# Kernel optimization log

Measured on AMD Instinct MI355X. Metric: run time of the kernel, lower is better.

## Reference

```python
import jax, jax.numpy as jnp
import numpy as np

N = 100000      # nodes (single ntype 'paper' for the reference)
R = 4           # relations
E = 300000      # edges per relation
P = 2           # prediction relations (pred_in_n_rev_etypes)
FEAT = 64       # feat_len
H = 64          # gen_h_dim
B = 2           # num_bases
NUM_PRED = 5
S = 4096        # seed nodes


def setup_inputs() -> dict:
    key = jax.random.key(0)
    ks = jax.random.split(key, 26)
    sc = 0.05
    inp = {
        "x": jax.random.normal(ks[0], (N, FEAT), jnp.float32),
        "edges": jax.random.randint(ks[1], (R, E, 2), 0, N, dtype=jnp.int32),
        "seeds": jax.random.randint(ks[2], (S,), 0, N, dtype=jnp.int32),
        "noise": jax.random.normal(ks[3], (N, H), jnp.float32),
        # RelGraphConv layer 1 (basis decomposition) and layer 2
        "V1": jax.random.normal(ks[4], (B, FEAT, H), jnp.float32) * sc,
        "C1": jax.random.normal(ks[5], (R, B), jnp.float32) * sc,
        "V2": jax.random.normal(ks[6], (B, H, H), jnp.float32) * sc,
        "C2": jax.random.normal(ks[7], (R, B), jnp.float32) * sc,
        # per-ntype linear head
        "W_lin": jax.random.normal(ks[8], (H, H), jnp.float32) * sc,
        "b_lin": jnp.zeros((H,), jnp.float32),
        # ReldGen per-relation MLP: H->256->32->1
        "Wd1": jax.random.normal(ks[9], (P, H, 256), jnp.float32) * sc,
        "bd1": jnp.zeros((P, 256), jnp.float32),
        "Wd2": jax.random.normal(ks[10], (P, 256, 32), jnp.float32) * sc,
        "bd2": jnp.zeros((P, 32), jnp.float32),
        "Wd3": jax.random.normal(ks[11], (P, 32, 1), jnp.float32) * sc,
        "bd3": jnp.zeros((P, 1), jnp.float32),
        # RelfGen per-relation MLP: H->256->2048->NUM_PRED*FEAT
        "Wf1": jax.random.normal(ks[12], (P, H, 256), jnp.float32) * sc,
        "bf1": jnp.zeros((P, 256), jnp.float32),
        "Wf2": jax.random.normal(ks[13], (P, 256, 2048), jnp.float32) * sc,
        "bf2": jnp.zeros((P, 2048), jnp.float32),
        "Wf3": jax.random.normal(ks[14], (P, 2048, NUM_PRED * FEAT), jnp.float32) * sc,
        "bf3": jnp.zeros((P, NUM_PRED * FEAT), jnp.float32),
    }
    return inp


def _rel_conv(h, V, C, edges):
    # basis decomposition: W_r = sum_b C[r,b] * V[b]
    Wr = jnp.einsum('rb,bio->rio', C, V)          # [R, in, out]
    m = jnp.einsum('ni,rio->rno', h, Wr)           # transform-then-gather

    def per_rel(m_r, e_r):
        msg = m_r[e_r[:, 0]]                       # gather src  [E, out]
        agg = jax.ops.segment_sum(msg, e_r[:, 1], num_segments=N)
        deg = jax.ops.segment_sum(jnp.ones((e_r.shape[0],), m_r.dtype),
                                  e_r[:, 1], num_segments=N)
        return agg / jnp.maximum(deg, 1.0)[:, None]  # GraphConv norm='right'

    out = jax.vmap(per_rel)(m, edges)              # [R, N, out]
    return jax.nn.relu(out.sum(axis=0))            # HeteroGraphConv 'sum' + relu


def reference(x, edges, seeds, noise, V1, C1, V2, C2, W_lin, b_lin,
              Wd1, bd1, Wd2, bd2, Wd3, bd3, Wf1, bf1, Wf2, bf2, Wf3, bf3):
    h = _rel_conv(x, V1, C1, edges)                # layer 1: FEAT -> H
    h = _rel_conv(h, V2, C2, edges)                # layer 2: H -> H
    h = jax.nn.leaky_relu(h @ W_lin + b_lin)       # per-ntype linear head
    h = h + noise                                  # Sampler: h + N(0,1)
    hs = h[seeds]                                  # [S, H]
    # ReldGen: predicted missing-neighbor counts per relation
    d = jax.nn.leaky_relu(jnp.einsum('sh,phk->psk', hs, Wd1) + bd1[:, None, :])
    d = jax.nn.leaky_relu(jnp.einsum('psk,pkm->psm', d, Wd2) + bd2[:, None, :])
    pred_missing = jax.nn.relu(jnp.einsum('psm,pmo->pso', d, Wd3) + bd3[:, None, :])  # [P,S,1]
    # RelfGen: predicted neighbor features per relation
    f = jax.nn.relu(jnp.einsum('sh,phk->psk', hs, Wf1) + bf1[:, None, :])
    f = jax.nn.relu(jnp.einsum('psk,pkm->psm', f, Wf2) + bf2[:, None, :])
    f = jnp.tanh(jnp.einsum('psm,pmo->pso', f, Wf3) + bf3[:, None, :])
    pred_feat = f.reshape(P, S, NUM_PRED, FEAT)
    return pred_missing, pred_feat
```

## Files before the change

kernel.cpp:

```cpp
#include <hip/hip_runtime.h>
#include <math.h>

#define NN 100000
#define RR 4
#define EE 300000
#define PP 2
#define HH 64
#define SS 4096
#define NSEG (NN * RR)
#define FPART 8
#define PWIDTH ((NN + FPART - 1) / FPART)

typedef __attribute__((ext_vector_type(8))) short short8;
typedef __attribute__((ext_vector_type(4))) short short4v;
typedef __attribute__((ext_vector_type(4))) float f32x4;

__device__ __forceinline__ short f2bf(float v) {
    unsigned u = __float_as_uint(v);
    unsigned r = (u + 0x7FFFu + ((u >> 16) & 1u)) >> 16;
    return (short)r;
}
__device__ __forceinline__ float bf2f(short s) {
    return __uint_as_float(((unsigned)(unsigned short)s) << 16);
}
__device__ __forceinline__ float bflo(unsigned v) { return __uint_as_float(v << 16); }
__device__ __forceinline__ float bfhi(unsigned v) { return __uint_as_float(v & 0xFFFF0000u); }

__global__ void compute_wr_t2(const float* __restrict__ C1, const float* __restrict__ V1,
                              short* __restrict__ hi1, short* __restrict__ lo1,
                              const float* __restrict__ C2, const float* __restrict__ V2,
                              short* __restrict__ hi2, short* __restrict__ lo2) {
    int b = blockIdx.x;
    const float* C = (b < 64) ? C1 : C2;
    const float* V = (b < 64) ? V1 : V2;
    short* hi = (b < 64) ? hi1 : hi2;
    short* lo = (b < 64) ? lo1 : lo2;
    int idx = (b & 63) * 256 + threadIdx.x;
    int o = idx >> 8;
    int ri = idx & 255;
    int r = ri >> 6;
    int i = ri & 63;
    float v = C[r * 2] * V[i * 64 + o] + C[r * 2 + 1] * V[4096 + i * 64 + o];
    short h = f2bf(v);
    hi[idx] = h;
    lo[idx] = f2bf(v - bf2f(h));
}

struct PrepPtrs {
    const float *Wlin, *Wd1, *Wd2, *Wf1, *Wf2, *Wf3;
    short *Wlin_hi, *Wlin_lo, *Wd1_hi, *Wd1_lo, *Wd2_hi, *Wd2_lo,
          *Wf1_hi, *Wf1_lo, *Wf2_hi, *Wf2_lo, *Wf3_hi, *Wf3_lo;
};

__device__ __forceinline__ void tsp_one(const float* __restrict__ W, short* __restrict__ hi,
                                        short* __restrict__ lo, int K, int N, int idx) {
    int total = K * N;
    int z = idx / total;
    int rem = idx - z * total;
    int n = rem / K;
    int k = rem - n * K;
    float v = W[(long long)z * total + (long long)k * N + n];
    short h = f2bf(v);
    hi[idx] = h;
    lo[idx] = f2bf(v - bf2f(h));
}

#define T0 4096
#define T1 32768
#define T2 16384
#define T3 32768
#define T4 1048576
#define T5 1310720
#define TSP_TOTAL (T0 + T1 + T2 + T3 + T4 + T5)

__global__ void prep_weights(PrepPtrs pp) {
    int idx = blockIdx.x * 256 + threadIdx.x;
    if (idx >= TSP_TOTAL) return;
    if (idx < T0) { tsp_one(pp.Wlin, pp.Wlin_hi, pp.Wlin_lo, 64, 64, idx); return; }
    idx -= T0;
    if (idx < T1) { tsp_one(pp.Wd1, pp.Wd1_hi, pp.Wd1_lo, 64, 256, idx); return; }
    idx -= T1;
    if (idx < T2) { tsp_one(pp.Wd2, pp.Wd2_hi, pp.Wd2_lo, 256, 32, idx); return; }
    idx -= T2;
    if (idx < T3) { tsp_one(pp.Wf1, pp.Wf1_hi, pp.Wf1_lo, 64, 256, idx); return; }
    idx -= T3;
    if (idx < T4) { tsp_one(pp.Wf2, pp.Wf2_hi, pp.Wf2_lo, 256, 2048, idx); return; }
    idx -= T4;
    tsp_one(pp.Wf3, pp.Wf3_hi, pp.Wf3_lo, 2048, 320, idx);
}

__global__ void to_bf16(const float* __restrict__ x, short* __restrict__ xb, int n4) {
    int idx = blockIdx.x * 256 + threadIdx.x;
    if (idx >= n4) return;
    f32x4 v = *(const f32x4*)&x[(long long)idx * 4];
    short4v o;
    #pragma unroll
    for (int c = 0; c < 4; c++) o[c] = f2bf(v[c]);
    *(short4v*)&xb[(long long)idx * 4] = o;
}

__global__ void count_kernel(const int* __restrict__ edges, int* __restrict__ counts) {
    int idx = blockIdx.x * 256 + threadIdx.x;
    if (idx >= RR * EE) return;
    int r = idx / EE;
    int dst = edges[2 * idx + 1];
    atomicAdd(&counts[dst * RR + r], 1);
}

__global__ void scan1(const int* __restrict__ counts, int* __restrict__ excl,
                      int* __restrict__ bsums, int n) {
    __shared__ int tmp[256];
    int tid = threadIdx.x;
    int gid = blockIdx.x * 256 + tid;
    int v = (gid < n) ? counts[gid] : 0;
    tmp[tid] = v;
    __syncthreads();
    #pragma unroll
    for (int off = 1; off < 256; off <<= 1) {
        int y = (tid >= off) ? tmp[tid - off] : 0;
        __syncthreads();
        tmp[tid] += y;
        __syncthreads();
    }
    if (gid < n) excl[gid] = tmp[tid] - v;
    if (tid == 255) bsums[blockIdx.x] = tmp[255];
}

__global__ void scan2(int* __restrict__ bsums, int nb) {
    __shared__ int tmp[256];
    __shared__ int carry;
    int tid = threadIdx.x;
    if (tid == 0) carry = 0;
    __syncthreads();
    for (int base = 0; base < nb; base += 256) {
        int i = base + tid;
        int v = (i < nb) ? bsums[i] : 0;
        tmp[tid] = v;
        __syncthreads();
        #pragma unroll
        for (int off = 1; off < 256; off <<= 1) {
            int y = (tid >= off) ? tmp[tid - off] : 0;
            __syncthreads();
            tmp[tid] += y;
            __syncthreads();
        }
        if (i < nb) bsums[i] = tmp[tid] - v + carry;
        __syncthreads();
        if (tid == 0) carry += tmp[255];
        __syncthreads();
    }
}

__global__ void scan3(const int* __restrict__ excl, const int* __restrict__ bsums,
                      int* __restrict__ row_ptr, int* __restrict__ cursor, int n, int total) {
    int gid = blockIdx.x * 256 + threadIdx.x;
    if (gid < n) {
        int v = excl[gid] + bsums[gid >> 8];
        row_ptr[gid] = v;
        cursor[gid] = v;
    }
    if (gid == 0) row_ptr[n] = total;
}

__global__ void fill_csr(const int* __restrict__ edges, int* __restrict__ cursor,
                         int* __restrict__ csr_src) {
    int part = blockIdx.x & (FPART - 1);
    int idx = (blockIdx.x >> 3) * 256 + threadIdx.x;
    if (idx >= RR * EE) return;
    int dst = edges[2 * idx + 1];
    int lo = part * PWIDTH;
    if (dst < lo || dst >= lo + PWIDTH) return;
    int r = idx / EE;
    int src = edges[2 * idx];
    int pos = atomicAdd(&cursor[dst * RR + r], 1);
    csr_src[pos] = src;
}

__global__ __launch_bounds__(256) void gather_agg(const int* __restrict__ row_ptr,
                                                  const int* __restrict__ csr_src,
                                                  const short* __restrict__ feat,
                                                  short* __restrict__ agg) {
    long long tg = (long long)blockIdx.x * 256 + threadIdx.x;
    long long seg = tg >> 5;
    int cl = threadIdx.x & 31;
    if (seg >= (long long)NSEG) return;
    int beg = row_ptr[seg];
    int end = row_ptr[seg + 1];
    float s0 = 0.f, s1 = 0.f;
    int i = beg;
    for (; i + 4 <= end; i += 4) {
        int a = csr_src[i];
        int b = csr_src[i + 1];
        int c = csr_src[i + 2];
        int d = csr_src[i + 3];
        unsigned va = *(const unsigned*)&feat[a * HH + cl * 2];
        unsigned vb = *(const unsigned*)&feat[b * HH + cl * 2];
        unsigned vc = *(const unsigned*)&feat[c * HH + cl * 2];
        unsigned vd = *(const unsigned*)&feat[d * HH + cl * 2];
        s0 += (bflo(va) + bflo(vb)) + (bflo(vc) + bflo(vd));
        s1 += (bfhi(va) + bfhi(vb)) + (bfhi(vc) + bfhi(vd));
    }
    int rem = end - i;
    if (rem > 0) {
        int a = csr_src[i];
        int b = csr_src[rem > 1 ? i + 1 : i];
        int c = csr_src[rem > 2 ? i + 2 : i];
        unsigned va = *(const unsigned*)&feat[a * HH + cl * 2];
        unsigned vb = *(const unsigned*)&feat[b * HH + cl * 2];
        unsigned vc = *(const unsigned*)&feat[c * HH + cl * 2];
        s0 += bflo(va);
        s1 += bfhi(va);
        s0 += (rem > 1) ? bflo(vb) : 0.f;
        s1 += (rem > 1) ? bfhi(vb) : 0.f;
        s0 += (rem > 2) ? bflo(vc) : 0.f;
        s1 += (rem > 2) ? bfhi(vc) : 0.f;
    }
    int d = end - beg;
    float inv = 1.0f / (float)(d > 1 ? d : 1);
    unsigned plo = (unsigned)(unsigned short)f2bf(s0 * inv);
    unsigned phi = (unsigned)(unsigned short)f2bf(s1 * inv);
    *(unsigned*)&agg[seg * HH + cl * 2] = plo | (phi << 16);
}

__global__ void gather_kernel(const float* __restrict__ h, const int* __restrict__ seeds,
                              float* __restrict__ hs) {
    int idx = blockIdx.x * 256 + threadIdx.x;
    if (idx >= SS * HH) return;
    int s = idx >> 6;
    hs[idx] = h[(long long)seeds[s] * HH + (idx & 63)];
}

__global__ void d3_kernel(const float* __restrict__ d2v, const float* __restrict__ Wd3,
                          const float* __restrict__ bd3, float* __restrict__ out) {
    int idx = blockIdx.x * 256 + threadIdx.x;
    if (idx >= PP * SS) return;
    int p = idx >> 12;
    const float* row = d2v + (long long)idx * 32;
    const float* w = Wd3 + p * 32;
    float s = bd3[p];
    #pragma unroll
    for (int k = 0; k < 32; k++) s += row[k] * w[k];
    out[idx] = fmaxf(s, 0.f);
}

__global__ void reduce_tanh(const float* __restrict__ part, const float* __restrict__ bf3,
                            float* __restrict__ out) {
    int idx = blockIdx.x * 256 + threadIdx.x;
    if (idx >= PP * SS * 320) return;
    int p = idx / (SS * 320);
    int rem = idx - p * (SS * 320);
    int n = rem % 320;
    float s = bf3[p * 320 + n];
    #pragma unroll
    for (int ks = 0; ks < 4; ks++)
        s += part[((long long)(p * 4 + ks)) * SS * 320 + rem];
    out[idx] = tanhf(s);
}

__global__ __launch_bounds__(256) void head1_gemm(
    const float* __restrict__ hs,
    const short* __restrict__ Bd_hi, const short* __restrict__ Bd_lo, const float* __restrict__ bd,
    const short* __restrict__ Bf_hi, const short* __restrict__ Bf_lo, const float* __restrict__ bfb,
    short* __restrict__ outd, short* __restrict__ outf)
{
    __shared__ short As_hi[128 * 32];
    __shared__ short As_lo[128 * 32];
    __shared__ short Bs_hi[64 * 32];
    __shared__ short Bs_lo[64 * 32];

    int z = blockIdx.z;
    int head = z >> 1, p = z & 1;
    const short* Bhi = (head ? Bf_hi : Bd_hi) + (long long)p * 256 * 64;
    const short* Blo = (head ? Bf_lo : Bd_lo) + (long long)p * 256 * 64;
    const float* bz = (head ? bfb : bd) + p * 256;
    short* Cc = (head ? outf : outd) + (long long)p * SS * 256;

    int m0 = blockIdx.y * 128;
    int n0 = blockIdx.x * 64;
    int tid = threadIdx.x;
    int lane = tid & 63;
    int w = tid >> 6;
    int wm = w >> 1, wn = w & 1;
    int mrow = lane & 15;
    int quad = lane >> 4;

    f32x4 acc[4][2];
    #pragma unroll
    for (int s = 0; s < 4; s++)
        #pragma unroll
        for (int t = 0; t < 2; t++)
            acc[s][t] = (f32x4){0.f, 0.f, 0.f, 0.f};

    #pragma unroll
    for (int k0 = 0; k0 < 64; k0 += 32) {
        #pragma unroll
        for (int i = 0; i < 4; i++) {
            int f = tid + i * 256;
            int m = f >> 3, k4 = f & 7;
            f32x4 v = *(const f32x4*)&hs[(m0 + m) * 64 + k0 + k4 * 4];
            short4v hv, lv;
            #pragma unroll
            for (int c = 0; c < 4; c++) {
                short hh = f2bf(v[c]);
                hv[c] = hh;
                lv[c] = f2bf(v[c] - bf2f(hh));
            }
            *(short4v*)&As_hi[m * 32 + k4 * 4] = hv;
            *(short4v*)&As_lo[m * 32 + k4 * 4] = lv;
        }
        {
            int n = tid >> 2, q = tid & 3;
            long long boff = (long long)(n0 + n) * 64 + k0 + q * 8;
            *(short8*)&Bs_hi[n * 32 + q * 8] = *(const short8*)&Bhi[boff];
            *(short8*)&Bs_lo[n * 32 + q * 8] = *(const short8*)&Blo[boff];
        }
        __syncthreads();

        short8 ah[4], al[4], bh[2], bl[2];
        #pragma unroll
        for (int s = 0; s < 4; s++) {
            int soff = (wm * 64 + s * 16 + mrow) * 32 + quad * 8;
            ah[s] = *(const short8*)&As_hi[soff];
            al[s] = *(const short8*)&As_lo[soff];
        }
        #pragma unroll
        for (int t = 0; t < 2; t++) {
            int soff = (wn * 32 + t * 16 + mrow) * 32 + quad * 8;
            bh[t] = *(const short8*)&Bs_hi[soff];
            bl[t] = *(const short8*)&Bs_lo[soff];
        }
        #pragma unroll
        for (int s = 0; s < 4; s++)
            #pragma unroll
            for (int t = 0; t < 2; t++) {
                acc[s][t] = __builtin_amdgcn_mfma_f32_16x16x32_bf16(ah[s], bh[t], acc[s][t], 0, 0, 0);
                acc[s][t] = __builtin_amdgcn_mfma_f32_16x16x32_bf16(ah[s], bl[t], acc[s][t], 0, 0, 0);
                acc[s][t] = __builtin_amdgcn_mfma_f32_16x16x32_bf16(al[s], bh[t], acc[s][t], 0, 0, 0);
            }
        __syncthreads();
    }

    #pragma unroll
    for (int s = 0; s < 4; s++) {
        int gmBase = m0 + wm * 64 + s * 16 + quad * 4;
        #pragma unroll
        for (int t = 0; t < 2; t++) {
            int gn = n0 + wn * 32 + t * 16 + mrow;
            float bb = bz[gn];
            #pragma unroll
            for (int r = 0; r < 4; r++) {
                int gm = gmBase + r;
                float v = acc[s][t][r] + bb;
                v = (head == 1) ? fmaxf(v, 0.f) : ((v > 0.f) ? v : 0.01f * v);
                Cc[(long long)gm * 256 + gn] = f2bf(v);
            }
        }
    }
}

template <int ACT, bool ADD, bool OUTBF, int KSPLIT>
__global__ __launch_bounds__(256) void mfma_gemm_bfA(
    const short* __restrict__ A, int lda, long long sA,
    const short* __restrict__ Bhi, const short* __restrict__ Blo, long long sB,
    const float* __restrict__ bias, long long sBias,
    const float* __restrict__ Dadd,
    void* __restrict__ Cc, int ldc, long long sC,
    int M, int Nn, int K)
{
    __shared__ short As[128 * 32];
    __shared__ short Bs_hi[64 * 32];
    __shared__ short Bs_lo[64 * 32];

    int z = blockIdx.z;
    int p = z / KSPLIT, ks = z % KSPLIT;
    A += (long long)p * sA;
    Bhi += (long long)p * sB;
    Blo += (long long)p * sB;
    const float* bz = bias ? bias + (long long)p * sBias : nullptr;
    long long cbase = (long long)((KSPLIT > 1) ? z : p) * sC;

    int Kc = K / KSPLIT;
    int kbeg = ks * Kc;

    int m0 = blockIdx.y * 128;
    int n0 = blockIdx.x * 64;
    int tid = threadIdx.x;
    int lane = tid & 63;
    int w = tid >> 6;
    int wm = w >> 1, wn = w & 1;
    int mrow = lane & 15;
    int quad = lane >> 4;

    f32x4 acc[4][2];
    #pragma unroll
    for (int s = 0; s < 4; s++)
        #pragma unroll
        for (int t = 0; t < 2; t++)
            acc[s][t] = (f32x4){0.f, 0.f, 0.f, 0.f};

    for (int k0 = kbeg; k0 < kbeg + Kc; k0 += 32) {
        #pragma unroll
        for (int i = 0; i < 2; i++) {
            int f = tid + i * 256;
            int m = f >> 2, q = f & 3;
            int gm = m0 + m;
            short8 av = (short8)0;
            if (gm < M) av = *(const short8*)&A[(long long)gm * lda + k0 + q * 8];
            *(short8*)&As[m * 32 + q * 8] = av;
        }
        {
            int n = tid >> 2, q = tid & 3;
            int gn = n0 + n;
            short8 bh = (short8)0, bl = (short8)0;
            if (gn < Nn) {
                long long boff = (long long)gn * K + k0 + q * 8;
                bh = *(const short8*)&Bhi[boff];
                bl = *(const short8*)&Blo[boff];
            }
            *(short8*)&Bs_hi[n * 32 + q * 8] = bh;
            *(short8*)&Bs_lo[n * 32 + q * 8] = bl;
        }
        __syncthreads();

        short8 ah[4], bh[2], bl[2];
        #pragma unroll
        for (int s = 0; s < 4; s++)
            ah[s] = *(const short8*)&As[(wm * 64 + s * 16 + mrow) * 32 + quad * 8];
        #pragma unroll
        for (int t = 0; t < 2; t++) {
            int soff = (wn * 32 + t * 16 + mrow) * 32 + quad * 8;
            bh[t] = *(const short8*)&Bs_hi[soff];
            bl[t] = *(const short8*)&Bs_lo[soff];
        }
        #pragma unroll
        for (int s = 0; s < 4; s++)
            #pragma unroll
            for (int t = 0; t < 2; t++) {
                acc[s][t] = __builtin_amdgcn_mfma_f32_16x16x32_bf16(ah[s], bh[t], acc[s][t], 0, 0, 0);
                acc[s][t] = __builtin_amdgcn_mfma_f32_16x16x32_bf16(ah[s], bl[t], acc[s][t], 0, 0, 0);
            }
        __syncthreads();
    }

    #pragma unroll
    for (int s = 0; s < 4; s++) {
        int gmBase = m0 + wm * 64 + s * 16 + quad * 4;
        #pragma unroll
        for (int t = 0; t < 2; t++) {
            int gn = n0 + wn * 32 + t * 16 + mrow;
            if (gn >= Nn) continue;
            float bb = bz ? bz[gn] : 0.f;
            #pragma unroll
            for (int r = 0; r < 4; r++) {
                int gm = gmBase + r;
                if (gm >= M) continue;
                float v = acc[s][t][r] + bb;
                if (ACT == 1) v = fmaxf(v, 0.f);
                else if (ACT == 2) v = (v > 0.f) ? v : 0.01f * v;
                else if (ACT == 3) v = tanhf(v);
                if (ADD) v += Dadd[(long long)gm * ldc + gn];
                long long co = cbase + (long long)gm * ldc + gn;
                if (OUTBF) ((short*)Cc)[co] = f2bf(v);
                else ((float*)Cc)[co] = v;
            }
        }
    }
}

extern "C" void kernel_launch(void* const* d_in, const int* in_sizes, int n_in,
                              void* d_out, int out_size, void* d_ws, size_t ws_size,
                              hipStream_t stream) {
    const float* x    = (const float*)d_in[0];
    const int* edges  = (const int*)d_in[1];
    const int* seeds  = (const int*)d_in[2];
    const float* noise= (const float*)d_in[3];
    const float* V1   = (const float*)d_in[4];
    const float* C1   = (const float*)d_in[5];
    const float* V2   = (const float*)d_in[6];
    const float* C2   = (const float*)d_in[7];
    const float* Wlin = (const float*)d_in[8];
    const float* blin = (const float*)d_in[9];
    const float* Wd1 = (const float*)d_in[10]; const float* bd1 = (const float*)d_in[11];
    const float* Wd2 = (const float*)d_in[12]; const float* bd2 = (const float*)d_in[13];
    const float* Wd3 = (const float*)d_in[14]; const float* bd3 = (const float*)d_in[15];
    const float* Wf1 = (const float*)d_in[16]; const float* bf1 = (const float*)d_in[17];
    const float* Wf2 = (const float*)d_in[18]; const float* bf2 = (const float*)d_in[19];
    const float* Wf3 = (const float*)d_in[20]; const float* bf3 = (const float*)d_in[21];

    float* out = (float*)d_out;

    char* ws = (char*)d_ws;
    size_t off = 0;
    auto allocf = [&](size_t nf) {
        float* p = (float*)(ws + off);
        off += ((nf * 4 + 255) / 256) * 256;
        return p;
    };
    auto allocs = [&](size_t ns) {
        short* p = (short*)(ws + off);
        off += ((ns * 2 + 255) / 256) * 256;
        return p;
    };
    auto alloci = [&](size_t ni) {
        int* p = (int*)(ws + off);
        off += ((ni * 4 + 255) / 256) * 256;
        return p;
    };

    short* Wrt1_hi = allocs(16384);          short* Wrt1_lo = allocs(16384);
    short* Wrt2_hi = allocs(16384);          short* Wrt2_lo = allocs(16384);
    short* Wlint_hi = allocs(4096);          short* Wlint_lo = allocs(4096);
    short* Wd1t_hi = allocs(2 * 64 * 256);   short* Wd1t_lo = allocs(2 * 64 * 256);
    short* Wd2t_hi = allocs(2 * 256 * 32);   short* Wd2t_lo = allocs(2 * 256 * 32);
    short* Wf1t_hi = allocs(2 * 64 * 256);   short* Wf1t_lo = allocs(2 * 64 * 256);
    short* Wf2t_hi = allocs((size_t)2 * 256 * 2048);  short* Wf2t_lo = allocs((size_t)2 * 256 * 2048);
    short* Wf3t_hi = allocs((size_t)2 * 2048 * 320);  short* Wf3t_lo = allocs((size_t)2 * 2048 * 320);

    int* counts  = alloci(NSEG);
    int* excl    = alloci(NSEG);
    int* bsums   = alloci(2048);
    int* row_ptr = alloci(NSEG + 1);
    int* cursor  = alloci(NSEG);
    int* csr_src = alloci((size_t)RR * EE);

    short* xb  = allocs((size_t)NN * HH);
    short* agg = allocs((size_t)NSEG * HH);
    short* h1  = allocs((size_t)NN * HH);
    short* h2  = allocs((size_t)NN * HH);
    float* h3  = allocf((size_t)NN * HH);
    float* hs  = allocf((size_t)SS * HH);
    short* d1b = allocs((size_t)PP * SS * 256);
    float* d2v = allocf((size_t)PP * SS * 32);
    short* f1  = allocs((size_t)PP * SS * 256);
    short* f2b = allocs((size_t)PP * SS * 2048);

    float* fpart = (float*)agg;

    compute_wr_t2<<<128, 256, 0, stream>>>(C1, V1, Wrt1_hi, Wrt1_lo, C2, V2, Wrt2_hi, Wrt2_lo);
    PrepPtrs pp;
    pp.Wlin = Wlin; pp.Wd1 = Wd1; pp.Wd2 = Wd2; pp.Wf1 = Wf1; pp.Wf2 = Wf2; pp.Wf3 = Wf3;
    pp.Wlin_hi = Wlint_hi; pp.Wlin_lo = Wlint_lo;
    pp.Wd1_hi = Wd1t_hi;   pp.Wd1_lo = Wd1t_lo;
    pp.Wd2_hi = Wd2t_hi;   pp.Wd2_lo = Wd2t_lo;
    pp.Wf1_hi = Wf1t_hi;   pp.Wf1_lo = Wf1t_lo;
    pp.Wf2_hi = Wf2t_hi;   pp.Wf2_lo = Wf2t_lo;
    pp.Wf3_hi = Wf3t_hi;   pp.Wf3_lo = Wf3t_lo;
    prep_weights<<<(TSP_TOTAL + 255) / 256, 256, 0, stream>>>(pp);

    to_bf16<<<(NN * HH / 4 + 255) / 256, 256, 0, stream>>>(x, xb, NN * HH / 4);

    hipMemsetAsync(counts, 0, (size_t)NSEG * 4, stream);
    int eb0 = (RR * EE + 255) / 256;
    count_kernel<<<eb0, 256, 0, stream>>>(edges, counts);
    int nb = (NSEG + 255) / 256;
    scan1<<<nb, 256, 0, stream>>>(counts, excl, bsums, NSEG);
    scan2<<<1, 256, 0, stream>>>(bsums, nb);
    scan3<<<nb, 256, 0, stream>>>(excl, bsums, row_ptr, cursor, NSEG, RR * EE);
    fill_csr<<<eb0 * FPART, 256, 0, stream>>>(edges, cursor, csr_src);

    int gb = (int)(((long long)NSEG * 32 + 255) / 256);
    int MY = (NN + 127) / 128;

    gather_agg<<<gb, 256, 0, stream>>>(row_ptr, csr_src, xb, agg);
    mfma_gemm_bfA<1, false, true, 1><<<dim3(1, MY, 1), 256, 0, stream>>>(
        agg, 256, 0, Wrt1_hi, Wrt1_lo, 0, nullptr, 0, nullptr,
        h1, 64, 0, NN, 64, 256);

    gather_agg<<<gb, 256, 0, stream>>>(row_ptr, csr_src, h1, agg);
    mfma_gemm_bfA<1, false, true, 1><<<dim3(1, MY, 1), 256, 0, stream>>>(
        agg, 256, 0, Wrt2_hi, Wrt2_lo, 0, nullptr, 0, nullptr,
        h2, 64, 0, NN, 64, 256);

    mfma_gemm_bfA<2, true, false, 1><<<dim3(1, MY, 1), 256, 0, stream>>>(
        h2, 64, 0, Wlint_hi, Wlint_lo, 0, blin, 0, noise,
        h3, 64, 0, NN, 64, 64);

    gather_kernel<<<(SS * HH + 255) / 256, 256, 0, stream>>>(h3, seeds, hs);

    head1_gemm<<<dim3(4, 32, 4), 256, 0, stream>>>(
        hs, Wd1t_hi, Wd1t_lo, bd1, Wf1t_hi, Wf1t_lo, bf1, d1b, f1);

    mfma_gemm_bfA<2, false, false, 1><<<dim3(1, 32, PP), 256, 0, stream>>>(
        d1b, 256, (long long)SS * 256, Wd2t_hi, Wd2t_lo, (long long)32 * 256, bd2, 32, nullptr,
        d2v, 32, (long long)SS * 32, SS, 32, 256);
    d3_kernel<<<(PP * SS + 255) / 256, 256, 0, stream>>>(d2v, Wd3, bd3, out);

    mfma_gemm_bfA<1, false, true, 1><<<dim3(32, 32, PP), 256, 0, stream>>>(
        f1, 256, (long long)SS * 256, Wf2t_hi, Wf2t_lo, (long long)2048 * 256, bf2, 2048, nullptr,
        f2b, 2048, (long long)SS * 2048, SS, 2048, 256);
    mfma_gemm_bfA<0, false, false, 4><<<dim3(5, 32, PP * 4), 256, 0, stream>>>(
        f2b, 2048, (long long)SS * 2048, Wf3t_hi, Wf3t_lo, (long long)320 * 2048, nullptr, 0, nullptr,
        fpart, 320, (long long)SS * 320, SS, 320, 2048);
    reduce_tanh<<<(PP * SS * 320 + 255) / 256, 256, 0, stream>>>(fpart, bf3, out + (size_t)PP * SS);
}
```

Baseline: 572.3 us.

## Fuse prep kernels, layer-2 GEMM with linear head, and d-head layers; widen gather loads

Three preprocessing kernels (basis weight combine, weight transpose/split, x to bf16) become one launch. The layer-2 relation GEMM is fused with the linear head, leaky ReLU and noise add through shared memory, so the h2 round trip disappears. The seed gather moves into head1, and the Wd2 GEMM is fused with the final Wd3 dot product. gather_agg now has 16 lanes per segment, each loading 8 bytes instead of 4. Together these cut launches and intermediate global traffic, at the cost of more shared memory per block in the fused kernels.

```diff
diff --git a/kernel.cpp b/kernel.cpp
--- a/kernel.cpp
+++ b/kernel.cpp
@@ -14,6 +14,7 @@
 typedef __attribute__((ext_vector_type(8))) short short8;
 typedef __attribute__((ext_vector_type(4))) short short4v;
 typedef __attribute__((ext_vector_type(4))) float f32x4;
+typedef __attribute__((ext_vector_type(2))) unsigned int u32x2;
 
 __device__ __forceinline__ short f2bf(float v) {
     unsigned u = __float_as_uint(v);
@@ -25,31 +26,18 @@
 }
 __device__ __forceinline__ float bflo(unsigned v) { return __uint_as_float(v << 16); }
 __device__ __forceinline__ float bfhi(unsigned v) { return __uint_as_float(v & 0xFFFF0000u); }
-
-__global__ void compute_wr_t2(const float* __restrict__ C1, const float* __restrict__ V1,
-                              short* __restrict__ hi1, short* __restrict__ lo1,
-                              const float* __restrict__ C2, const float* __restrict__ V2,
-                              short* __restrict__ hi2, short* __restrict__ lo2) {
-    int b = blockIdx.x;
-    const float* C = (b < 64) ? C1 : C2;
-    const float* V = (b < 64) ? V1 : V2;
-    short* hi = (b < 64) ? hi1 : hi2;
-    short* lo = (b < 64) ? lo1 : lo2;
-    int idx = (b & 63) * 256 + threadIdx.x;
-    int o = idx >> 8;
-    int ri = idx & 255;
-    int r = ri >> 6;
-    int i = ri & 63;
-    float v = C[r * 2] * V[i * 64 + o] + C[r * 2 + 1] * V[4096 + i * 64 + o];
-    short h = f2bf(v);
-    hi[idx] = h;
-    lo[idx] = f2bf(v - bf2f(h));
+__device__ __forceinline__ unsigned pack2(float a, float b) {
+    return (unsigned)(unsigned short)f2bf(a) | ((unsigned)(unsigned short)f2bf(b) << 16);
 }
 
 struct PrepPtrs {
     const float *Wlin, *Wd1, *Wd2, *Wf1, *Wf2, *Wf3;
     short *Wlin_hi, *Wlin_lo, *Wd1_hi, *Wd1_lo, *Wd2_hi, *Wd2_lo,
           *Wf1_hi, *Wf1_lo, *Wf2_hi, *Wf2_lo, *Wf3_hi, *Wf3_lo;
+    const float *C1, *V1, *C2, *V2;
+    short *wr1_hi, *wr1_lo, *wr2_hi, *wr2_lo;
+    const float *x;
+    short *xb;
 };
 
 __device__ __forceinline__ void tsp_one(const float* __restrict__ W, short* __restrict__ hi,
@@ -72,31 +60,51 @@
 #define T4 1048576
 #define T5 1310720
 #define TSP_TOTAL (T0 + T1 + T2 + T3 + T4 + T5)
-
-__global__ void prep_weights(PrepPtrs pp) {
-    int idx = blockIdx.x * 256 + threadIdx.x;
-    if (idx >= TSP_TOTAL) return;
-    if (idx < T0) { tsp_one(pp.Wlin, pp.Wlin_hi, pp.Wlin_lo, 64, 64, idx); return; }
-    idx -= T0;
-    if (idx < T1) { tsp_one(pp.Wd1, pp.Wd1_hi, pp.Wd1_lo, 64, 256, idx); return; }
-    idx -= T1;
-    if (idx < T2) { tsp_one(pp.Wd2, pp.Wd2_hi, pp.Wd2_lo, 256, 32, idx); return; }
-    idx -= T2;
-    if (idx < T3) { tsp_one(pp.Wf1, pp.Wf1_hi, pp.Wf1_lo, 64, 256, idx); return; }
-    idx -= T3;
-    if (idx < T4) { tsp_one(pp.Wf2, pp.Wf2_hi, pp.Wf2_lo, 256, 2048, idx); return; }
-    idx -= T4;
-    tsp_one(pp.Wf3, pp.Wf3_hi, pp.Wf3_lo, 2048, 320, idx);
-}
-
-__global__ void to_bf16(const float* __restrict__ x, short* __restrict__ xb, int n4) {
-    int idx = blockIdx.x * 256 + threadIdx.x;
-    if (idx >= n4) return;
-    f32x4 v = *(const f32x4*)&x[(long long)idx * 4];
+#define WR_BLK 128
+#define TSP_BLK 9552
+#define XB_BLK 6250
+
+__global__ void prep_all(PrepPtrs pp) {
+    int b = blockIdx.x;
+    if (b < WR_BLK) {
+        const float* C = (b < 64) ? pp.C1 : pp.C2;
+        const float* V = (b < 64) ? pp.V1 : pp.V2;
+        short* hi = (b < 64) ? pp.wr1_hi : pp.wr2_hi;
+        short* lo = (b < 64) ? pp.wr1_lo : pp.wr2_lo;
+        int idx = (b & 63) * 256 + threadIdx.x;
+        int o = idx >> 8;
+        int ri = idx & 255;
+        int r = ri >> 6;
+        int i = ri & 63;
+        float v = C[r * 2] * V[i * 64 + o] + C[r * 2 + 1] * V[4096 + i * 64 + o];
+        short h = f2bf(v);
+        hi[idx] = h;
+        lo[idx] = f2bf(v - bf2f(h));
+        return;
+    }
+    b -= WR_BLK;
+    if (b < TSP_BLK) {
+        int idx = b * 256 + threadIdx.x;
+        if (idx < T0) { tsp_one(pp.Wlin, pp.Wlin_hi, pp.Wlin_lo, 64, 64, idx); return; }
+        idx -= T0;
+        if (idx < T1) { tsp_one(pp.Wd1, pp.Wd1_hi, pp.Wd1_lo, 64, 256, idx); return; }
+        idx -= T1;
+        if (idx < T2) { tsp_one(pp.Wd2, pp.Wd2_hi, pp.Wd2_lo, 256, 32, idx); return; }
+        idx -= T2;
+        if (idx < T3) { tsp_one(pp.Wf1, pp.Wf1_hi, pp.Wf1_lo, 64, 256, idx); return; }
+        idx -= T3;
+        if (idx < T4) { tsp_one(pp.Wf2, pp.Wf2_hi, pp.Wf2_lo, 256, 2048, idx); return; }
+        idx -= T4;
+        tsp_one(pp.Wf3, pp.Wf3_hi, pp.Wf3_lo, 2048, 320, idx);
+        return;
+    }
+    b -= TSP_BLK;
+    int idx = b * 256 + threadIdx.x;
+    f32x4 v = *(const f32x4*)&pp.x[(long long)idx * 4];
     short4v o;
     #pragma unroll
     for (int c = 0; c < 4; c++) o[c] = f2bf(v[c]);
-    *(short4v*)&xb[(long long)idx * 4] = o;
+    *(short4v*)&pp.xb[(long long)idx * 4] = o;
 }
 
 __global__ void count_kernel(const int* __restrict__ edges, int* __restrict__ counts) {
@@ -181,66 +189,45 @@
                                                   const short* __restrict__ feat,
                                                   short* __restrict__ agg) {
     long long tg = (long long)blockIdx.x * 256 + threadIdx.x;
-    long long seg = tg >> 5;
-    int cl = threadIdx.x & 31;
+    long long seg = tg >> 4;
+    int cl = threadIdx.x & 15;
     if (seg >= (long long)NSEG) return;
     int beg = row_ptr[seg];
     int end = row_ptr[seg + 1];
-    float s0 = 0.f, s1 = 0.f;
+    float s0 = 0.f, s1 = 0.f, s2 = 0.f, s3 = 0.f;
     int i = beg;
     for (; i + 4 <= end; i += 4) {
         int a = csr_src[i];
         int b = csr_src[i + 1];
         int c = csr_src[i + 2];
         int d = csr_src[i + 3];
-        unsigned va = *(const unsigned*)&feat[a * HH + cl * 2];
-        unsigned vb = *(const unsigned*)&feat[b * HH + cl * 2];
-        unsigned vc = *(const unsigned*)&feat[c * HH + cl * 2];
-        unsigned vd = *(const unsigned*)&feat[d * HH + cl * 2];
-        s0 += (bflo(va) + bflo(vb)) + (bflo(vc) + bflo(vd));
-        s1 += (bfhi(va) + bfhi(vb)) + (bfhi(vc) + bfhi(vd));
+        u32x2 va = *(const u32x2*)&feat[a * HH + cl * 4];
+        u32x2 vb = *(const u32x2*)&feat[b * HH + cl * 4];
+        u32x2 vc = *(const u32x2*)&feat[c * HH + cl * 4];
+        u32x2 vd = *(const u32x2*)&feat[d * HH + cl * 4];
+        s0 += (bflo(va.x) + bflo(vb.x)) + (bflo(vc.x) + bflo(vd.x));
+        s1 += (bfhi(va.x) + bfhi(vb.x)) + (bfhi(vc.x) + bfhi(vd.x));
+        s2 += (bflo(va.y) + bflo(vb.y)) + (bflo(vc.y) + bflo(vd.y));
+        s3 += (bfhi(va.y) + bfhi(vb.y)) + (bfhi(vc.y) + bfhi(vd.y));
     }
     int rem = end - i;
     if (rem > 0) {
         int a = csr_src[i];
         int b = csr_src[rem > 1 ? i + 1 : i];
         int c = csr_src[rem > 2 ? i + 2 : i];
-        unsigned va = *(const unsigned*)&feat[a * HH + cl * 2];
-        unsigned vb = *(const unsigned*)&feat[b * HH + cl * 2];
-        unsigned vc = *(const unsigned*)&feat[c * HH + cl * 2];
-        s0 += bflo(va);
-        s1 += bfhi(va);
-        s0 += (rem > 1) ? bflo(vb) : 0.f;
-        s1 += (rem > 1) ? bfhi(vb) : 0.f;
-        s0 += (rem > 2) ? bflo(vc) : 0.f;
-        s1 += (rem > 2) ? bfhi(vc) : 0.f;
+        u32x2 va = *(const u32x2*)&feat[a * HH + cl * 4];
+        u32x2 vb = *(const u32x2*)&feat[b * HH + cl * 4];
+        u32x2 vc = *(const u32x2*)&feat[c * HH + cl * 4];
+        s0 += bflo(va.x); s1 += bfhi(va.x); s2 += bflo(va.y); s3 += bfhi(va.y);
+        if (rem > 1) { s0 += bflo(vb.x); s1 += bfhi(vb.x); s2 += bflo(vb.y); s3 += bfhi(vb.y); }
+        if (rem > 2) { s0 += bflo(vc.x); s1 += bfhi(vc.x); s2 += bflo(vc.y); s3 += bfhi(vc.y); }
     }
     int d = end - beg;
     float inv = 1.0f / (float)(d > 1 ? d : 1);
-    unsigned plo = (unsigned)(unsigned short)f2bf(s0 * inv);
-    unsigned phi = (unsigned)(unsigned short)f2bf(s1 * inv);
-    *(unsigned*)&agg[seg * HH + cl * 2] = plo | (phi << 16);
-}
-
-__global__ void gather_kernel(const float* __restrict__ h, const int* __restrict__ seeds,
-                              float* __restrict__ hs) {
-    int idx = blockIdx.x * 256 + threadIdx.x;
-    if (idx >= SS * HH) return;
-    int s = idx >> 6;
-    hs[idx] = h[(long long)seeds[s] * HH + (idx & 63)];
-}
-
-__global__ void d3_kernel(const float* __restrict__ d2v, const float* __restrict__ Wd3,
-                          const float* __restrict__ bd3, float* __restrict__ out) {
-    int idx = blockIdx.x * 256 + threadIdx.x;
-    if (idx >= PP * SS) return;
-    int p = idx >> 12;
-    const float* row = d2v + (long long)idx * 32;
-    const float* w = Wd3 + p * 32;
-    float s = bd3[p];
-    #pragma unroll
-    for (int k = 0; k < 32; k++) s += row[k] * w[k];
-    out[idx] = fmaxf(s, 0.f);
+    u32x2 outp;
+    outp.x = pack2(s0 * inv, s1 * inv);
+    outp.y = pack2(s2 * inv, s3 * inv);
+    *(u32x2*)&agg[seg * HH + cl * 4] = outp;
 }
 
 __global__ void reduce_tanh(const float* __restrict__ part, const float* __restrict__ bf3,
@@ -257,8 +244,250 @@
     out[idx] = tanhf(s);
 }
 
+template <int ACT, bool OUTBF, int KSPLIT>
+__global__ __launch_bounds__(256) void mfma_gemm_bfA(
+    const short* __restrict__ A, int lda, long long sA,
+    const short* __restrict__ Bhi, const short* __restrict__ Blo, long long sB,
+    const float* __restrict__ bias, long long sBias,
+    void* __restrict__ Cc, int ldc, long long sC,
+    int M, int Nn, int K)
+{
+    __shared__ short As[128 * 32];
+    __shared__ short Bs_hi[64 * 32];
+    __shared__ short Bs_lo[64 * 32];
+
+    int z = blockIdx.z;
+    int p = z / KSPLIT, ks = z % KSPLIT;
+    A += (long long)p * sA;
+    Bhi += (long long)p * sB;
+    Blo += (long long)p * sB;
+    const float* bz = bias ? bias + (long long)p * sBias : nullptr;
+    long long cbase = (long long)((KSPLIT > 1) ? z : p) * sC;
+
+    int Kc = K / KSPLIT;
+    int kbeg = ks * Kc;
+
+    int m0 = blockIdx.y * 128;
+    int n0 = blockIdx.x * 64;
+    int tid = threadIdx.x;
+    int lane = tid & 63;
+    int w = tid >> 6;
+    int wm = w >> 1, wn = w & 1;
+    int mrow = lane & 15;
+    int quad = lane >> 4;
+
+    f32x4 acc[4][2];
+    #pragma unroll
+    for (int s = 0; s < 4; s++)
+        #pragma unroll
+        for (int t = 0; t < 2; t++)
+            acc[s][t] = (f32x4){0.f, 0.f, 0.f, 0.f};
+
+    for (int k0 = kbeg; k0 < kbeg + Kc; k0 += 32) {
+        #pragma unroll
+        for (int i = 0; i < 2; i++) {
+            int f = tid + i * 256;
+            int m = f >> 2, q = f & 3;
+            int gm = m0 + m;
+            short8 av = (short8)0;
+            if (gm < M) av = *(const short8*)&A[(long long)gm * lda + k0 + q * 8];
+            *(short8*)&As[m * 32 + q * 8] = av;
+        }
+        {
+            int n = tid >> 2, q = tid & 3;
+            int gn = n0 + n;
+            short8 bh = (short8)0, bl = (short8)0;
+            if (gn < Nn) {
+                long long boff = (long long)gn * K + k0 + q * 8;
+                bh = *(const short8*)&Bhi[boff];
+                bl = *(const short8*)&Blo[boff];
+            }
+            *(short8*)&Bs_hi[n * 32 + q * 8] = bh;
+            *(short8*)&Bs_lo[n * 32 + q * 8] = bl;
+        }
+        __syncthreads();
+
+        short8 ah[4], bh[2], bl[2];
+        #pragma unroll
+        for (int s = 0; s < 4; s++)
+            ah[s] = *(const short8*)&As[(wm * 64 + s * 16 + mrow) * 32 + quad * 8];
+        #pragma unroll
+        for (int t = 0; t < 2; t++) {
+            int soff = (wn * 32 + t * 16 + mrow) * 32 + quad * 8;
+            bh[t] = *(const short8*)&Bs_hi[soff];
+            bl[t] = *(const short8*)&Bs_lo[soff];
+        }
+        #pragma unroll
+        for (int s = 0; s < 4; s++)
+            #pragma unroll
+            for (int t = 0; t < 2; t++) {
+                acc[s][t] = __builtin_amdgcn_mfma_f32_16x16x32_bf16(ah[s], bh[t], acc[s][t], 0, 0, 0);
+                acc[s][t] = __builtin_amdgcn_mfma_f32_16x16x32_bf16(ah[s], bl[t], acc[s][t], 0, 0, 0);
+            }
+        __syncthreads();
+    }
+
+    #pragma unroll
+    for (int s = 0; s < 4; s++) {
+        int gmBase = m0 + wm * 64 + s * 16 + quad * 4;
+        #pragma unroll
+        for (int t = 0; t < 2; t++) {
+            int gn = n0 + wn * 32 + t * 16 + mrow;
+            if (gn >= Nn) continue;
+            float bb = bz ? bz[gn] : 0.f;
+            #pragma unroll
+            for (int r = 0; r < 4; r++) {
+                int gm = gmBase + r;
+                if (gm >= M) continue;
+                float v = acc[s][t][r] + bb;
+                if (ACT == 1) v = fmaxf(v, 0.f);
+                else if (ACT == 2) v = (v > 0.f) ? v : 0.01f * v;
+                long long co = cbase + (long long)gm * ldc + gn;
+                if (OUTBF) ((short*)Cc)[co] = f2bf(v);
+                else ((float*)Cc)[co] = v;
+            }
+        }
+    }
+}
+
+__global__ __launch_bounds__(256) void combine2_linear(
+    const short* __restrict__ A,
+    const short* __restrict__ Bhi, const short* __restrict__ Blo,
+    const short* __restrict__ Lhi, const short* __restrict__ Llo,
+    const float* __restrict__ blin, const float* __restrict__ noise,
+    float* __restrict__ h3)
+{
+    __shared__ short As[128 * 32];
+    __shared__ short Bs_hi[64 * 32];
+    __shared__ short Bs_lo[64 * 32];
+    __shared__ short Ls_hi[64 * 64];
+    __shared__ short Ls_lo[64 * 64];
+    __shared__ short h2s[128 * 64];
+
+    int tid = threadIdx.x;
+    int lane = tid & 63;
+    int w = tid >> 6;
+    int wm = w >> 1, wn = w & 1;
+    int mrow = lane & 15;
+    int quad = lane >> 4;
+    int m0 = blockIdx.x * 128;
+
+    {
+        int base = tid * 16;
+        *(short8*)&Ls_hi[base] = *(const short8*)&Lhi[base];
+        *(short8*)&Ls_hi[base + 8] = *(const short8*)&Lhi[base + 8];
+        *(short8*)&Ls_lo[base] = *(const short8*)&Llo[base];
+        *(short8*)&Ls_lo[base + 8] = *(const short8*)&Llo[base + 8];
+    }
+
+    f32x4 acc[4][2];
+    #pragma unroll
+    for (int s = 0; s < 4; s++)
+        #pragma unroll
+        for (int t = 0; t < 2; t++)
+            acc[s][t] = (f32x4){0.f, 0.f, 0.f, 0.f};
+
+    for (int k0 = 0; k0 < 256; k0 += 32) {
+        #pragma unroll
+        for (int i = 0; i < 2; i++) {
+            int f = tid + i * 256;
+            int m = f >> 2, q = f & 3;
+            int gm = m0 + m;
+            short8 av = (short8)0;
+            if (gm < NN) av = *(const short8*)&A[(long long)gm * 256 + k0 + q * 8];
+            *(short8*)&As[m * 32 + q * 8] = av;
+        }
+        {
+            int n = tid >> 2, q = tid & 3;
+            long long boff = (long long)n * 256 + k0 + q * 8;
+            *(short8*)&Bs_hi[n * 32 + q * 8] = *(const short8*)&Bhi[boff];
+            *(short8*)&Bs_lo[n * 32 + q * 8] = *(const short8*)&Blo[boff];
+        }
+        __syncthreads();
+
+        short8 ah[4], bh[2], bl[2];
+        #pragma unroll
+        for (int s = 0; s < 4; s++)
+            ah[s] = *(const short8*)&As[(wm * 64 + s * 16 + mrow) * 32 + quad * 8];
+        #pragma unroll
+        for (int t = 0; t < 2; t++) {
+            int soff = (wn * 32 + t * 16 + mrow) * 32 + quad * 8;
+            bh[t] = *(const short8*)&Bs_hi[soff];
+            bl[t] = *(const short8*)&Bs_lo[soff];
+        }
+        #pragma unroll
+        for (int s = 0; s < 4; s++)
+            #pragma unroll
+            for (int t = 0; t < 2; t++) {
+                acc[s][t] = __builtin_amdgcn_mfma_f32_16x16x32_bf16(ah[s], bh[t], acc[s][t], 0, 0, 0);
+                acc[s][t] = __builtin_amdgcn_mfma_f32_16x16x32_bf16(ah[s], bl[t], acc[s][t], 0, 0, 0);
+            }
+        __syncthreads();
+    }
+
+    #pragma unroll
+    for (int s = 0; s < 4; s++) {
+        int rowB = wm * 64 + s * 16 + quad * 4;
+        #pragma unroll
+        for (int t = 0; t < 2; t++) {
+            int col = wn * 32 + t * 16 + mrow;
+            #pragma unroll
+            for (int r = 0; r < 4; r++)
+                h2s[(rowB + r) * 64 + col] = f2bf(fmaxf(acc[s][t][r], 0.f));
+        }
+    }
+    __syncthreads();
+
+    f32x4 acc2[4][2];
+    #pragma unroll
+    for (int s = 0; s < 4; s++)
+        #pragma unroll
+        for (int t = 0; t < 2; t++)
+            acc2[s][t] = (f32x4){0.f, 0.f, 0.f, 0.f};
+
+    #pragma unroll
+    for (int k0 = 0; k0 < 64; k0 += 32) {
+        short8 ah[4], bh[2], bl[2];
+        #pragma unroll
+        for (int s = 0; s < 4; s++)
+            ah[s] = *(const short8*)&h2s[(wm * 64 + s * 16 + mrow) * 64 + k0 + quad * 8];
+        #pragma unroll
+        for (int t = 0; t < 2; t++) {
+            int soff = (wn * 32 + t * 16 + mrow) * 64 + k0 + quad * 8;
+            bh[t] = *(const short8*)&Ls_hi[soff];
+            bl[t] = *(const short8*)&Ls_lo[soff];
+        }
+        #pragma unroll
+        for (int s = 0; s < 4; s++)
+            #pragma unroll
+            for (int t = 0; t < 2; t++) {
+                acc2[s][t] = __builtin_amdgcn_mfma_f32_16x16x32_bf16(ah[s], bh[t], acc2[s][t], 0, 0, 0);
+                acc2[s][t] = __builtin_amdgcn_mfma_f32_16x16x32_bf16(ah[s], bl[t], acc2[s][t], 0, 0, 0);
+            }
+    }
+
+    #pragma unroll
+    for (int s = 0; s < 4; s++) {
+        int gmBase = m0 + wm * 64 + s * 16 + quad * 4;
+        #pragma unroll
+        for (int t = 0; t < 2; t++) {
+            int gn = wn * 32 + t * 16 + mrow;
+            float bb = blin[gn];
+            #pragma unroll
+            for (int r = 0; r < 4; r++) {
+                int gm = gmBase + r;
+                if (gm >= NN) continue;
+                float v = acc2[s][t][r] + bb;
+                v = (v > 0.f) ? v : 0.01f * v;
+                v += noise[(long long)gm * 64 + gn];
+                h3[(long long)gm * 64 + gn] = v;
+            }
+        }
+    }
+}
+
 __global__ __launch_bounds__(256) void head1_gemm(
-    const float* __restrict__ hs,
+    const float* __restrict__ h3, const int* __restrict__ seeds,
     const short* __restrict__ Bd_hi, const short* __restrict__ Bd_lo, const float* __restrict__ bd,
     const short* __restrict__ Bf_hi, const short* __restrict__ Bf_lo, const float* __restrict__ bfb,
     short* __restrict__ outd, short* __restrict__ outf)
@@ -297,7 +526,8 @@
         for (int i = 0; i < 4; i++) {
             int f = tid + i * 256;
             int m = f >> 3, k4 = f & 7;
-            f32x4 v = *(const f32x4*)&hs[(m0 + m) * 64 + k0 + k4 * 4];
+            int node = seeds[m0 + m];
+            f32x4 v = *(const f32x4*)&h3[(long long)node * 64 + k0 + k4 * 4];
             short4v hv, lv;
             #pragma unroll
             for (int c = 0; c < 4; c++) {
@@ -358,32 +588,23 @@
     }
 }
 
-template <int ACT, bool ADD, bool OUTBF, int KSPLIT>
-__global__ __launch_bounds__(256) void mfma_gemm_bfA(
-    const short* __restrict__ A, int lda, long long sA,
-    const short* __restrict__ Bhi, const short* __restrict__ Blo, long long sB,
-    const float* __restrict__ bias, long long sBias,
-    const float* __restrict__ Dadd,
-    void* __restrict__ Cc, int ldc, long long sC,
-    int M, int Nn, int K)
+__global__ __launch_bounds__(256) void dhead_gemm(
+    const short* __restrict__ d1b,
+    const short* __restrict__ Bhi, const short* __restrict__ Blo,
+    const float* __restrict__ bd2, const float* __restrict__ Wd3,
+    const float* __restrict__ bd3, float* __restrict__ out)
 {
     __shared__ short As[128 * 32];
     __shared__ short Bs_hi[64 * 32];
     __shared__ short Bs_lo[64 * 32];
-
-    int z = blockIdx.z;
-    int p = z / KSPLIT, ks = z % KSPLIT;
-    A += (long long)p * sA;
-    Bhi += (long long)p * sB;
-    Blo += (long long)p * sB;
-    const float* bz = bias ? bias + (long long)p * sBias : nullptr;
-    long long cbase = (long long)((KSPLIT > 1) ? z : p) * sC;
-
-    int Kc = K / KSPLIT;
-    int kbeg = ks * Kc;
+    __shared__ float d2s[128][33];
+
+    int p = blockIdx.z;
+    const short* A = d1b + (long long)p * SS * 256;
+    const short* Bh = Bhi + (long long)p * 32 * 256;
+    const short* Bl = Blo + (long long)p * 32 * 256;
 
     int m0 = blockIdx.y * 128;
-    int n0 = blockIdx.x * 64;
     int tid = threadIdx.x;
     int lane = tid & 63;
     int w = tid >> 6;
@@ -398,24 +619,20 @@
         for (int t = 0; t < 2; t++)
             acc[s][t] = (f32x4){0.f, 0.f, 0.f, 0.f};
 
-    for (int k0 = kbeg; k0 < kbeg + Kc; k0 += 32) {
+    for (int k0 = 0; k0 < 256; k0 += 32) {
         #pragma unroll
         for (int i = 0; i < 2; i++) {
             int f = tid + i * 256;
             int m = f >> 2, q = f & 3;
-            int gm = m0 + m;
-            short8 av = (short8)0;
-            if (gm < M) av = *(const short8*)&A[(long long)gm * lda + k0 + q * 8];
-            *(short8*)&As[m * 32 + q * 8] = av;
+            *(short8*)&As[m * 32 + q * 8] = *(const short8*)&A[(long long)(m0 + m) * 256 + k0 + q * 8];
         }
         {
             int n = tid >> 2, q = tid & 3;
-            int gn = n0 + n;
             short8 bh = (short8)0, bl = (short8)0;
-            if (gn < Nn) {
-                long long boff = (long long)gn * K + k0 + q * 8;
-                bh = *(const short8*)&Bhi[boff];
-                bl = *(const short8*)&Blo[boff];
+            if (n < 32) {
+                long long boff = (long long)n * 256 + k0 + q * 8;
+                bh = *(const short8*)&Bh[boff];
+                bl = *(const short8*)&Bl[boff];
             }
             *(short8*)&Bs_hi[n * 32 + q * 8] = bh;
             *(short8*)&Bs_lo[n * 32 + q * 8] = bl;
@@ -442,28 +659,28 @@
         __syncthreads();
     }
 
-    #pragma unroll
-    for (int s = 0; s < 4; s++) {
-        int gmBase = m0 + wm * 64 + s * 16 + quad * 4;
-        #pragma unroll
-        for (int t = 0; t < 2; t++) {
-            int gn = n0 + wn * 32 + t * 16 + mrow;
-            if (gn >= Nn) continue;
-            float bb = bz ? bz[gn] : 0.f;
-            #pragma unroll
-            for (int r = 0; r < 4; r++) {
-                int gm = gmBase + r;
-                if (gm >= M) continue;
-                float v = acc[s][t][r] + bb;
-                if (ACT == 1) v = fmaxf(v, 0.f);
-                else if (ACT == 2) v = (v > 0.f) ? v : 0.01f * v;
-                else if (ACT == 3) v = tanhf(v);
-                if (ADD) v += Dadd[(long long)gm * ldc + gn];
-                long long co = cbase + (long long)gm * ldc + gn;
-                if (OUTBF) ((short*)Cc)[co] = f2bf(v);
-                else ((float*)Cc)[co] = v;
-            }
-        }
+    if (wn == 0) {
+        #pragma unroll
+        for (int s = 0; s < 4; s++) {
+            int rowB = wm * 64 + s * 16 + quad * 4;
+            #pragma unroll
+            for (int t = 0; t < 2; t++) {
+                int col = t * 16 + mrow;
+                #pragma unroll
+                for (int r = 0; r < 4; r++) {
+                    float v = acc[s][t][r] + bd2[p * 32 + col];
+                    d2s[rowB + r][col] = (v > 0.f) ? v : 0.01f * v;
+                }
+            }
+        }
+    }
+    __syncthreads();
+
+    if (tid < 128) {
+        float sacc = bd3[p];
+        #pragma unroll
+        for (int k = 0; k < 32; k++) sacc += d2s[tid][k] * Wd3[p * 32 + k];
+        out[p * SS + m0 + tid] = fmaxf(sacc, 0.f);
     }
 }
 
@@ -526,17 +743,13 @@
     short* xb  = allocs((size_t)NN * HH);
     short* agg = allocs((size_t)NSEG * HH);
     short* h1  = allocs((size_t)NN * HH);
-    short* h2  = allocs((size_t)NN * HH);
     float* h3  = allocf((size_t)NN * HH);
-    float* hs  = allocf((size_t)SS * HH);
     short* d1b = allocs((size_t)PP * SS * 256);
-    float* d2v = allocf((size_t)PP * SS * 32);
     short* f1  = allocs((size_t)PP * SS * 256);
     short* f2b = allocs((size_t)PP * SS * 2048);
 
     float* fpart = (float*)agg;
 
-    compute_wr_t2<<<128, 256, 0, stream>>>(C1, V1, Wrt1_hi, Wrt1_lo, C2, V2, Wrt2_hi, Wrt2_lo);
     PrepPtrs pp;
     pp.Wlin = Wlin; pp.Wd1 = Wd1; pp.Wd2 = Wd2; pp.Wf1 = Wf1; pp.Wf2 = Wf2; pp.Wf3 = Wf3;
     pp.Wlin_hi = Wlint_hi; pp.Wlin_lo = Wlint_lo;
@@ -545,9 +758,10 @@
     pp.Wf1_hi = Wf1t_hi;   pp.Wf1_lo = Wf1t_lo;
     pp.Wf2_hi = Wf2t_hi;   pp.Wf2_lo = Wf2t_lo;
     pp.Wf3_hi = Wf3t_hi;   pp.Wf3_lo = Wf3t_lo;
-    prep_weights<<<(TSP_TOTAL + 255) / 256, 256, 0, stream>>>(pp);
-
-    to_bf16<<<(NN * HH / 4 + 255) / 256, 256, 0, stream>>>(x, xb, NN * HH / 4);
+    pp.C1 = C1; pp.V1 = V1; pp.C2 = C2; pp.V2 = V2;
+    pp.wr1_hi = Wrt1_hi; pp.wr1_lo = Wrt1_lo; pp.wr2_hi = Wrt2_hi; pp.wr2_lo = Wrt2_lo;
+    pp.x = x; pp.xb = xb;
+    prep_all<<<WR_BLK + TSP_BLK + XB_BLK, 256, 0, stream>>>(pp);
 
     hipMemsetAsync(counts, 0, (size_t)NSEG * 4, stream);
     int eb0 = (RR * EE + 255) / 256;
@@ -558,38 +772,29 @@
     scan3<<<nb, 256, 0, stream>>>(excl, bsums, row_ptr, cursor, NSEG, RR * EE);
     fill_csr<<<eb0 * FPART, 256, 0, stream>>>(edges, cursor, csr_src);
 
-    int gb = (int)(((long long)NSEG * 32 + 255) / 256);
+    int gb = (int)(((long long)NSEG * 16 + 255) / 256);
     int MY = (NN + 127) / 128;
 
     gather_agg<<<gb, 256, 0, stream>>>(row_ptr, csr_src, xb, agg);
-    mfma_gemm_bfA<1, false, true, 1><<<dim3(1, MY, 1), 256, 0, stream>>>(
-        agg, 256, 0, Wrt1_hi, Wrt1_lo, 0, nullptr, 0, nullptr,
+    mfma_gemm_bfA<1, true, 1><<<dim3(1, MY, 1), 256, 0, stream>>>(
+        agg, 256, 0, Wrt1_hi, Wrt1_lo, 0, nullptr, 0,
         h1, 64, 0, NN, 64, 256);
 
     gather_agg<<<gb, 256, 0, stream>>>(row_ptr, csr_src, h1, agg);
-    mfma_gemm_bfA<1, false, true, 1><<<dim3(1, MY, 1), 256, 0, stream>>>(
-        agg, 256, 0, Wrt2_hi, Wrt2_lo, 0, nullptr, 0, nullptr,
-        h2, 64, 0, NN, 64, 256);
-
-    mfma_gemm_bfA<2, true, false, 1><<<dim3(1, MY, 1), 256, 0, stream>>>(
-        h2, 64, 0, Wlint_hi, Wlint_lo, 0, blin, 0, noise,
-        h3, 64, 0, NN, 64, 64);
-
-    gather_kernel<<<(SS * HH + 255) / 256, 256, 0, stream>>>(h3, seeds, hs);
+    combine2_linear<<<MY, 256, 0, stream>>>(
+        agg, Wrt2_hi, Wrt2_lo, Wlint_hi, Wlint_lo, blin, noise, h3);
 
     head1_gemm<<<dim3(4, 32, 4), 256, 0, stream>>>(
-        hs, Wd1t_hi, Wd1t_lo, bd1, Wf1t_hi, Wf1t_lo, bf1, d1b, f1);
-
-    mfma_gemm_bfA<2, false, false, 1><<<dim3(1, 32, PP), 256, 0, stream>>>(
-        d1b, 256, (long long)SS * 256, Wd2t_hi, Wd2t_lo, (long long)32 * 256, bd2, 32, nullptr,
-        d2v, 32, (long long)SS * 32, SS, 32, 256);
-    d3_kernel<<<(PP * SS + 255) / 256, 256, 0, stream>>>(d2v, Wd3, bd3, out);
-
-    mfma_gemm_bfA<1, false, true, 1><<<dim3(32, 32, PP), 256, 0, stream>>>(
-        f1, 256, (long long)SS * 256, Wf2t_hi, Wf2t_lo, (long long)2048 * 256, bf2, 2048, nullptr,
+        h3, seeds, Wd1t_hi, Wd1t_lo, bd1, Wf1t_hi, Wf1t_lo, bf1, d1b, f1);
+
+    dhead_gemm<<<dim3(1, 32, PP), 256, 0, stream>>>(
+        d1b, Wd2t_hi, Wd2t_lo, bd2, Wd3, bd3, out);
+
+    mfma_gemm_bfA<1, true, 1><<<dim3(32, 32, PP), 256, 0, stream>>>(
+        f1, 256, (long long)SS * 256, Wf2t_hi, Wf2t_lo, (long long)2048 * 256, bf2, 2048,
         f2b, 2048, (long long)SS * 2048, SS, 2048, 256);
-    mfma_gemm_bfA<0, false, false, 4><<<dim3(5, 32, PP * 4), 256, 0, stream>>>(
-        f2b, 2048, (long long)SS * 2048, Wf3t_hi, Wf3t_lo, (long long)320 * 2048, nullptr, 0, nullptr,
+    mfma_gemm_bfA<0, false, 4><<<dim3(5, 32, PP * 4), 256, 0, stream>>>(
+        f2b, 2048, (long long)SS * 2048, Wf3t_hi, Wf3t_lo, (long long)320 * 2048, nullptr, 0,
         fpart, 320, (long long)SS * 320, SS, 320, 2048);
     reduce_tanh<<<(PP * SS * 320 + 255) / 256, 256, 0, stream>>>(fpart, bf3, out + (size_t)PP * SS);
 }
```

Result: faster. 529.1 us (-7.5%).
